# Performance work log

Hardware: AMD Instinct MI355X
Metric: run time of the kernel (lower is better)

Reference implementation:

```python
import jax, jax.numpy as jnp
import numpy as np

EPS = 1e-6
N_HEADS = 8


def causal_dot_product(q, k, v):
    # q,k: [n,h,l,d]; v: [n,h,l,m]
    kv = jnp.einsum('nhld,nhlm->nhldm', k, v)          # [n,h,l,d,m] (large, matches original)
    kv = jnp.cumsum(kv, axis=2)
    return jnp.einsum('nhld,nhldm->nhlm', q, kv)


def flow_attention_causal(queries, keys, values, Wq, bq, Wk, bk, Wv, bv, Wo, bo):
    B, L, _ = queries.shape
    H = N_HEADS
    # projections + split heads -> [B,H,L,Dh]
    def proj(x, W, b):
        y = x @ W + b
        return y.reshape(B, L, H, -1).transpose(0, 2, 1, 3)
    q = jax.nn.sigmoid(proj(queries, Wq, bq))
    k = jax.nn.sigmoid(proj(keys, Wk, bk))
    v = proj(values, Wv, bv)

    normal = (jnp.arange(L, dtype=q.dtype) + 1.0)[None, None, :]  # [1,1,L]

    sink_incoming = 1.0 / jnp.einsum('nhld,nhld->nhl', q + EPS, jnp.cumsum(k, axis=2) + EPS)
    source_outgoing = 1.0 / jnp.einsum('nhld,nhld->nhl', k + EPS, jnp.cumsum(q, axis=2) + EPS)
    sink_incoming = sink_incoming * normal
    source_outgoing = source_outgoing * normal

    conserved_sink = jnp.einsum('nhld,nhld->nhl', q + EPS,
                                jnp.cumsum(k * source_outgoing[..., None], axis=2) + EPS) / normal
    conserved_source = jnp.einsum('nhld,nhld->nhl', k + EPS,
                                  jnp.cumsum(q * sink_incoming[..., None], axis=2) + EPS) / normal
    conserved_source = jnp.clip(conserved_source, -1.0, 1.0)

    sink_allocation = jax.nn.sigmoid(conserved_sink)
    conserved_source = jnp.exp(conserved_source)
    source_competition = conserved_source / jnp.cumsum(conserved_source, axis=-1) * normal

    x = causal_dot_product(q * (sink_incoming / normal)[..., None],
                           k,
                           v * source_competition[..., None]) * sink_allocation[..., None]
    x = x.transpose(0, 2, 1, 3).reshape(B, L, -1)
    return x @ Wo + bo  # dropout is identity at eval


def setup_inputs() -> dict:
    key = jax.random.key(0)
    ks = jax.random.split(key, 11)
    B, L, Din, Dm, Dout = 2, 1024, 512, 512, 512
    s = 0.02
    return {
        'queries': jax.random.normal(ks[0], (B, L, Din), jnp.float32),
        'keys': jax.random.normal(ks[1], (B, L, Din), jnp.float32),
        'values': jax.random.normal(ks[2], (B, L, Din), jnp.float32),
        'Wq': jax.random.normal(ks[3], (Din, Dm), jnp.float32) * s,
        'bq': jnp.zeros((Dm,), jnp.float32),
        'Wk': jax.random.normal(ks[4], (Din, Dm), jnp.float32) * s,
        'bk': jnp.zeros((Dm,), jnp.float32),
        'Wv': jax.random.normal(ks[5], (Din, Dm), jnp.float32) * s,
        'bv': jnp.zeros((Dm,), jnp.float32),
        'Wo': jax.random.normal(ks[6], (Dm, Dout), jnp.float32) * s,
        'bo': jnp.zeros((Dout,), jnp.float32),
    }


def reference(queries, keys, values, Wq, bq, Wk, bk, Wv, bv, Wo, bo):
    return flow_attention_causal(queries, keys, values, Wq, bq, Wk, bk, Wv, bv, Wo, bo)
```

## Files before the change

kernel.cpp:

```cpp
#include <hip/hip_runtime.h>
#include <math.h>

#define EPSF 1e-6f

constexpr int B_  = 2;
constexpr int L_  = 1024;
constexpr int D_  = 512;
constexpr int H_  = 8;
constexpr int DH_ = 64;
constexpr int BL_ = B_ * L_;
constexpr int BH_ = B_ * H_;
constexpr int CT_ = 64;
constexpr int NC_ = L_ / CT_;

typedef __attribute__((ext_vector_type(8))) short bf16x8;
typedef __attribute__((ext_vector_type(4))) float f32x4;

__device__ __forceinline__ unsigned short f2bf(float f) {
  union { float f; unsigned int u; } v; v.f = f;
  const unsigned int u = v.u;
  return (unsigned short)((u + 0x7FFFu + ((u >> 16) & 1u)) >> 16);
}

__device__ __forceinline__ int sw(int row, int col) {
  return row * 64 + (col ^ ((row & 7) << 3));
}

__global__ __launch_bounds__(256) void proj3_k(const float* __restrict__ Qin,
                                               const float* __restrict__ Kin,
                                               const float* __restrict__ Vin,
                                               const float* __restrict__ Wq,
                                               const float* __restrict__ bq,
                                               const float* __restrict__ Wk,
                                               const float* __restrict__ bk,
                                               const float* __restrict__ Wv,
                                               const float* __restrict__ bv,
                                               float* __restrict__ Qb,
                                               float* __restrict__ Kb,
                                               float* __restrict__ Vb,
                                               float* __restrict__ sumQ,
                                               float* __restrict__ sumK) {
  const int z = blockIdx.z;
  const float* A    = (z == 0) ? Qin : (z == 1) ? Kin : Vin;
  const float* W    = (z == 0) ? Wq  : (z == 1) ? Wk  : Wv;
  const float* bias = (z == 0) ? bq  : (z == 1) ? bk  : bv;
  float* out        = (z == 0) ? Qb  : (z == 1) ? Kb  : Vb;
  float* csum       = (z == 0) ? sumQ : (z == 1) ? sumK : nullptr;
  const bool sig = (z < 2);

  __shared__ __align__(16) short Als[64 * 40];
  __shared__ __align__(16) short Bls[64 * 40];
  const int tid = threadIdx.x;
  const int m0 = blockIdx.x * 64, n0 = blockIdx.y * 64;
  const int arow = tid >> 2, akq = (tid & 3) << 3;
  const int bcol = tid & 63, bk0 = (tid >> 6) << 3;
  const int lane = tid & 63, wid = tid >> 6;
  const int wr = wid >> 1, wc = wid & 1;
  const int lrow = lane & 15, lk = (lane >> 4) << 3;

  f32x4 acc[2][2] = {{{0.f, 0.f, 0.f, 0.f}, {0.f, 0.f, 0.f, 0.f}},
                     {{0.f, 0.f, 0.f, 0.f}, {0.f, 0.f, 0.f, 0.f}}};
  float ra[8], rb[8];

  auto loadAB = [&](int kt) {
    const float4 f0 = *(const float4*)&A[(size_t)(m0 + arow) * D_ + kt + akq];
    const float4 f1 = *(const float4*)&A[(size_t)(m0 + arow) * D_ + kt + akq + 4];
    ra[0] = f0.x; ra[1] = f0.y; ra[2] = f0.z; ra[3] = f0.w;
    ra[4] = f1.x; ra[5] = f1.y; ra[6] = f1.z; ra[7] = f1.w;
    const float* gw = &W[(size_t)(kt + bk0) * D_ + n0 + bcol];
#pragma unroll
    for (int j = 0; j < 8; ++j) rb[j] = gw[(size_t)j * D_];
  };
  auto writeLDS = [&]() {
    bf16x8 pa, pb;
#pragma unroll
    for (int j = 0; j < 8; ++j) {
      pa[j] = (short)f2bf(ra[j]);
      pb[j] = (short)f2bf(rb[j]);
    }
    *(bf16x8*)&Als[arow * 40 + akq] = pa;
    *(bf16x8*)&Bls[bcol * 40 + bk0] = pb;
  };
  auto compute = [&]() {
    bf16x8 a0 = *(const bf16x8*)&Als[(wr * 32 + lrow) * 40 + lk];
    bf16x8 a1 = *(const bf16x8*)&Als[(wr * 32 + 16 + lrow) * 40 + lk];
    bf16x8 b0 = *(const bf16x8*)&Bls[(wc * 32 + lrow) * 40 + lk];
    bf16x8 b1 = *(const bf16x8*)&Bls[(wc * 32 + 16 + lrow) * 40 + lk];
    acc[0][0] = __builtin_amdgcn_mfma_f32_16x16x32_bf16(a0, b0, acc[0][0], 0, 0, 0);
    acc[0][1] = __builtin_amdgcn_mfma_f32_16x16x32_bf16(a0, b1, acc[0][1], 0, 0, 0);
    acc[1][0] = __builtin_amdgcn_mfma_f32_16x16x32_bf16(a1, b0, acc[1][0], 0, 0, 0);
    acc[1][1] = __builtin_amdgcn_mfma_f32_16x16x32_bf16(a1, b1, acc[1][1], 0, 0, 0);
  };

  loadAB(0);
  writeLDS();
  for (int kt = 32; kt < D_; kt += 32) {
    loadAB(kt);
    __syncthreads();
    compute();
    __syncthreads();
    writeLDS();
  }
  __syncthreads();
  compute();

  const int b = m0 >> 10, h = n0 >> 6;
  float psum[2] = {0.f, 0.f};
#pragma unroll
  for (int j = 0; j < 2; ++j) {
    const int col = n0 + wc * 32 + j * 16 + lrow;
    const float bv4 = bias[col];
    const int dh = col & 63;
#pragma unroll
    for (int i = 0; i < 2; ++i) {
#pragma unroll
      for (int r = 0; r < 4; ++r) {
        const int row = m0 + wr * 32 + i * 16 + (lane >> 4) * 4 + r;
        float x = acc[i][j][r] + bv4;
        if (sig) x = 1.0f / (1.0f + expf(-x));
        const int l = row & (L_ - 1);
        out[(((size_t)(b * H_ + h)) * L_ + l) * DH_ + dh] = x;
        psum[j] += x;
      }
    }
  }
  if (csum) {
    float* sumS = (float*)Als;
#pragma unroll
    for (int j = 0; j < 2; ++j) {
      psum[j] += __shfl_xor(psum[j], 16);
      psum[j] += __shfl_xor(psum[j], 32);
      if ((lane >> 4) == 0) sumS[wr * 64 + wc * 32 + j * 16 + lrow] = psum[j];
    }
    __syncthreads();
    if (tid < 64) {
      const int c = (m0 & (L_ - 1)) >> 6;
      const int bc = (b * H_ + h) * NC_ + c;
      csum[bc * DH_ + tid] = sumS[tid] + sumS[64 + tid];
    }
  }
}

__global__ __launch_bounds__(256) void flow_phase1_k(const float* __restrict__ Qb,
                                                     const float* __restrict__ Kb,
                                                     const float* __restrict__ sumQ,
                                                     const float* __restrict__ sumK,
                                                     float* __restrict__ qscale,
                                                     float* __restrict__ si_a,
                                                     float* __restrict__ so_a,
                                                     float* __restrict__ sumQSI,
                                                     float* __restrict__ sumKSO) {
  const int bc = blockIdx.x, bh = bc >> 4, c = bc & (NC_ - 1);
  const int g = bc * CT_;
  const int tid = threadIdx.x, lane = tid & 63, w = tid >> 6;
  __shared__ float qS[64][65], kS[64][65];
  __shared__ float pqS[64], pkS[64];
  __shared__ float aS[4][64], bS[4][64];
  __shared__ float siS[64], soS[64];
  for (int i = tid; i < CT_ * DH_; i += 256) {
    const int row = i >> 6, d = i & 63;
    qS[row][d] = Qb[(size_t)g * DH_ + i];
    kS[row][d] = Kb[(size_t)g * DH_ + i];
  }
  if (tid < 64) {
    float pq = 0.f, pk = 0.f;
    for (int cc = 0; cc < c; ++cc) {
      pq += sumQ[(bh * NC_ + cc) * DH_ + tid];
      pk += sumK[(bh * NC_ + cc) * DH_ + tid];
    }
    pqS[tid] = pq; pkS[tid] = pk;
  }
  __syncthreads();
  float ap = 0.f, bp = 0.f;
  for (int dd = 0; dd < 16; ++dd) {
    const int d = w * 16 + dd;
    const float qv = qS[lane][d];
    const float kv = kS[lane][d];
    float ck = kv, cq = qv;
#pragma unroll
    for (int off = 1; off < 64; off <<= 1) {
      const float t1 = __shfl_up(ck, off);
      const float t2 = __shfl_up(cq, off);
      ck += (lane >= off) ? t1 : 0.f;
      cq += (lane >= off) ? t2 : 0.f;
    }
    ck += pkS[d];
    cq += pqS[d];
    ap += (qv + EPSF) * (ck + EPSF);
    bp += (kv + EPSF) * (cq + EPSF);
  }
  aS[w][lane] = ap; bS[w][lane] = bp;
  __syncthreads();
  const float normal = (float)(c * CT_ + lane + 1);
  if (w == 0) {
    const float a = aS[0][lane] + aS[1][lane] + aS[2][lane] + aS[3][lane];
    const float b = bS[0][lane] + bS[1][lane] + bS[2][lane] + bS[3][lane];
    const float si = normal / a, so = normal / b;
    qscale[g + lane] = 1.0f / a;
    si_a[g + lane] = si;
    so_a[g + lane] = so;
    siS[lane] = si; soS[lane] = so;
  }
  __syncthreads();
  float sq = 0.f, sk = 0.f;
#pragma unroll
  for (int li = 0; li < 16; ++li) {
    const int l = w * 16 + li;
    sq += qS[l][lane] * siS[l];
    sk += kS[l][lane] * soS[l];
  }
  aS[w][lane] = sq; bS[w][lane] = sk;
  __syncthreads();
  if (tid < 64) {
    sumQSI[bc * DH_ + tid] = aS[0][tid] + aS[1][tid] + aS[2][tid] + aS[3][tid];
    sumKSO[bc * DH_ + tid] = bS[0][tid] + bS[1][tid] + bS[2][tid] + bS[3][tid];
  }
}

__global__ __launch_bounds__(256) void flow_phase2_k(const float* __restrict__ Qb,
                                                     const float* __restrict__ Kb,
                                                     const float* __restrict__ sumQSI,
                                                     const float* __restrict__ sumKSO,
                                                     const float* __restrict__ si_a,
                                                     const float* __restrict__ so_a,
                                                     float* __restrict__ salloc,
                                                     float* __restrict__ e_a,
                                                     float* __restrict__ sumE) {
  const int bc = blockIdx.x, bh = bc >> 4, c = bc & (NC_ - 1);
  const int g = bc * CT_;
  const int tid = threadIdx.x, lane = tid & 63, w = tid >> 6;
  __shared__ float qS[64][65], kS[64][65];
  __shared__ float pqS[64], pkS[64];
  __shared__ float aS[4][64], bS[4][64];
  for (int i = tid; i < CT_ * DH_; i += 256) {
    const int row = i >> 6, d = i & 63;
    qS[row][d] = Qb[(size_t)g * DH_ + i];
    kS[row][d] = Kb[(size_t)g * DH_ + i];
  }
  if (tid < 64) {
    float pq = 0.f, pk = 0.f;
    for (int cc = 0; cc < c; ++cc) {
      pq += sumQSI[(bh * NC_ + cc) * DH_ + tid];
      pk += sumKSO[(bh * NC_ + cc) * DH_ + tid];
    }
    pqS[tid] = pq; pkS[tid] = pk;
  }
  __syncthreads();
  const float si = si_a[g + lane];
  const float so = so_a[g + lane];
  float c1p = 0.f, c2p = 0.f;
  for (int dd = 0; dd < 16; ++dd) {
    const int d = w * 16 + dd;
    const float qv = qS[lane][d];
    const float kv = kS[lane][d];
    float ckso = kv * so, cqsi = qv * si;
#pragma unroll
    for (int off = 1; off < 64; off <<= 1) {
      const float t1 = __shfl_up(ckso, off);
      const float t2 = __shfl_up(cqsi, off);
      ckso += (lane >= off) ? t1 : 0.f;
      cqsi += (lane >= off) ? t2 : 0.f;
    }
    ckso += pkS[d];
    cqsi += pqS[d];
    c1p += (qv + EPSF) * (ckso + EPSF);
    c2p += (kv + EPSF) * (cqsi + EPSF);
  }
  aS[w][lane] = c1p; bS[w][lane] = c2p;
  __syncthreads();
  if (w == 0) {
    const float c1 = aS[0][lane] + aS[1][lane] + aS[2][lane] + aS[3][lane];
    const float c2 = bS[0][lane] + bS[1][lane] + bS[2][lane] + bS[3][lane];
    const float normal = (float)(c * CT_ + lane + 1);
    const float cs_sink = c1 / normal;
    salloc[g + lane] = 1.0f / (1.0f + expf(-cs_sink));
    float cs_src = c2 / normal;
    cs_src = fminf(1.0f, fmaxf(-1.0f, cs_src));
    const float e = expf(cs_src);
    e_a[g + lane] = e;
    float tot = e;
#pragma unroll
    for (int off = 32; off; off >>= 1) tot += __shfl_xor(tot, off);
    if (lane == 0) sumE[bc] = tot;
  }
}

__global__ __launch_bounds__(256) void flow_ckv_k(const float* __restrict__ K,
                                                  const float* __restrict__ V,
                                                  const float* __restrict__ e_a,
                                                  const float* __restrict__ sumE,
                                                  float* __restrict__ comp,
                                                  float* __restrict__ KV) {
  const int bc = blockIdx.x, bh = bc >> 4, c = bc & (NC_ - 1);
  const int g = bc * CT_;
  const int tid = threadIdx.x;
  __shared__ float compS[CT_];
  __shared__ float kb[CT_][DH_];
  __shared__ float vb[CT_][DH_];
  if (tid < 64) {
    const int lane = tid;
    const float e = e_a[g + lane];
    float se = (lane < c) ? sumE[bh * NC_ + lane] : 0.f;
#pragma unroll
    for (int off = 32; off; off >>= 1) se += __shfl_xor(se, off);
    float s = e;
#pragma unroll
    for (int off = 1; off < 64; off <<= 1) {
      const float t = __shfl_up(s, off);
      s += (lane >= off) ? t : 0.f;
    }
    const float cf = e / (se + s) * (float)(c * CT_ + lane + 1);
    compS[lane] = cf;
    comp[g + lane] = cf;
  }
  __syncthreads();
  const float* k = K + (size_t)g * DH_;
  const float* v = V + (size_t)g * DH_;
  for (int i = tid; i < CT_ * DH_; i += 256) {
    const int l = i >> 6;
    kb[l][i & 63] = k[i];
    vb[l][i & 63] = v[i] * compS[l];
  }
  __syncthreads();
  const int m = tid & 63, dg = tid >> 6;
  float acc[16] = {};
  for (int l = 0; l < CT_; ++l) {
    const float vm = vb[l][m];
#pragma unroll
    for (int i = 0; i < 16; ++i) acc[i] += kb[l][dg * 16 + i] * vm;
  }
  float* out = KV + ((size_t)bc * DH_ + dg * 16) * DH_ + m;
#pragma unroll
  for (int i = 0; i < 16; ++i) out[i * DH_] = acc[i];
}

__global__ __launch_bounds__(256) void kv_prefix_k(float* __restrict__ KV) {
  const int idx = blockIdx.x * 256 + threadIdx.x;
  const int bh = idx >> 12, p = idx & 4095;
  const size_t base = (size_t)bh * NC_ * DH_ * DH_ + p;
  float run = 0.f;
#pragma unroll
  for (int c = 0; c < NC_; ++c) {
    const float t = KV[base + (size_t)c * DH_ * DH_];
    KV[base + (size_t)c * DH_ * DH_] = run;
    run += t;
  }
}

__global__ __launch_bounds__(256) void attn_k(const float* __restrict__ Q,
                                              const float* __restrict__ K,
                                              const float* __restrict__ V,
                                              const float* __restrict__ KVp,
                                              const float* __restrict__ qscale,
                                              const float* __restrict__ salloc,
                                              const float* __restrict__ comp,
                                              unsigned short* __restrict__ X) {
  const int bc = blockIdx.x;
  const int bh = bc >> 4, c = bc & (NC_ - 1);
  const int bb = bh >> 3, hh = bh & (H_ - 1);
  const int g = bc * CT_;
  __shared__ __align__(16) unsigned short qp16[64 * 64];
  __shared__ __align__(16) unsigned short k16[64 * 64];
  __shared__ __align__(16) unsigned short vT16[64 * 64];
  __shared__ __align__(16) unsigned short kvT16[64 * 64];
  __shared__ __align__(16) unsigned short S16[64 * 64];
  const int tid = threadIdx.x;
  for (int i = tid; i < 64 * 64; i += 256) {
    const int r = i >> 6, d = i & 63;
    qp16[sw(r, d)] = f2bf(Q[(size_t)g * DH_ + i] * qscale[g + r]);
    k16[sw(r, d)] = f2bf(K[(size_t)g * DH_ + i]);
    vT16[sw(d, r)] = f2bf(V[(size_t)g * DH_ + i] * comp[g + r]);
    kvT16[sw(d, r)] = f2bf(KVp[(size_t)bc * DH_ * DH_ + i]);
  }
  __syncthreads();

  const int lane = tid & 63, w = tid >> 6;
  const int fr = lane & 15, fk = (lane >> 4) << 3;
  const int arow = w * 16 + fr;
  f32x4 accX[4] = {{0.f, 0.f, 0.f, 0.f}, {0.f, 0.f, 0.f, 0.f},
                   {0.f, 0.f, 0.f, 0.f}, {0.f, 0.f, 0.f, 0.f}};
  f32x4 accS[4] = {{0.f, 0.f, 0.f, 0.f}, {0.f, 0.f, 0.f, 0.f},
                   {0.f, 0.f, 0.f, 0.f}, {0.f, 0.f, 0.f, 0.f}};

  const bf16x8 aq0 = *(const bf16x8*)&qp16[sw(arow, fk)];
  const bf16x8 aq1 = *(const bf16x8*)&qp16[sw(arow, fk + 32)];
#pragma unroll
  for (int cb = 0; cb < 4; ++cb) {
    const int bcol = cb * 16 + fr;
    const bf16x8 bv0 = *(const bf16x8*)&kvT16[sw(bcol, fk)];
    const bf16x8 bv1 = *(const bf16x8*)&kvT16[sw(bcol, fk + 32)];
    accX[cb] = __builtin_amdgcn_mfma_f32_16x16x32_bf16(aq0, bv0, accX[cb], 0, 0, 0);
    accX[cb] = __builtin_amdgcn_mfma_f32_16x16x32_bf16(aq1, bv1, accX[cb], 0, 0, 0);
    const bf16x8 bk0 = *(const bf16x8*)&k16[sw(bcol, fk)];
    const bf16x8 bk1 = *(const bf16x8*)&k16[sw(bcol, fk + 32)];
    accS[cb] = __builtin_amdgcn_mfma_f32_16x16x32_bf16(aq0, bk0, accS[cb], 0, 0, 0);
    accS[cb] = __builtin_amdgcn_mfma_f32_16x16x32_bf16(aq1, bk1, accS[cb], 0, 0, 0);
  }
#pragma unroll
  for (int cb = 0; cb < 4; ++cb) {
#pragma unroll
    for (int r = 0; r < 4; ++r) {
      const int l = w * 16 + (lane >> 4) * 4 + r;
      const int j = cb * 16 + fr;
      S16[sw(l, j)] = (j <= l) ? f2bf(accS[cb][r]) : (unsigned short)0;
    }
  }
  __syncthreads();
  const bf16x8 as0 = *(const bf16x8*)&S16[sw(arow, fk)];
  const bf16x8 as1 = *(const bf16x8*)&S16[sw(arow, fk + 32)];
#pragma unroll
  for (int cb = 0; cb < 4; ++cb) {
    const int bcol = cb * 16 + fr;
    const bf16x8 bv0 = *(const bf16x8*)&vT16[sw(bcol, fk)];
    const bf16x8 bv1 = *(const bf16x8*)&vT16[sw(bcol, fk + 32)];
    accX[cb] = __builtin_amdgcn_mfma_f32_16x16x32_bf16(as0, bv0, accX[cb], 0, 0, 0);
    accX[cb] = __builtin_amdgcn_mfma_f32_16x16x32_bf16(as1, bv1, accX[cb], 0, 0, 0);
  }
#pragma unroll
  for (int r = 0; r < 4; ++r) {
    const int l = w * 16 + (lane >> 4) * 4 + r;
    const float sal = salloc[g + l];
    const size_t rowbase = ((size_t)(bb * L_ + c * CT_ + l)) * D_ + hh * DH_;
#pragma unroll
    for (int cb = 0; cb < 4; ++cb) {
      const int m = cb * 16 + fr;
      X[rowbase + m] = f2bf(accX[cb][r] * sal);
    }
  }
}

__global__ __launch_bounds__(256) void gemm_out_k(const unsigned short* __restrict__ A,
                                                  const float* __restrict__ W,
                                                  const float* __restrict__ bias,
                                                  float* __restrict__ out) {
  __shared__ __align__(16) short Als[64 * 40];
  __shared__ __align__(16) short Bls[64 * 40];
  const int tid = threadIdx.x;
  const int m0 = blockIdx.x * 64, n0 = blockIdx.y * 64;
  const int arow = tid >> 2, akq = (tid & 3) << 3;
  const int bcol = tid & 63, bk0 = (tid >> 6) << 3;
  const int lane = tid & 63, wid = tid >> 6;
  const int wr = wid >> 1, wc = wid & 1;
  const int lrow = lane & 15, lk = (lane >> 4) << 3;

  f32x4 acc[2][2] = {{{0.f, 0.f, 0.f, 0.f}, {0.f, 0.f, 0.f, 0.f}},
                     {{0.f, 0.f, 0.f, 0.f}, {0.f, 0.f, 0.f, 0.f}}};
  bf16x8 pa;
  float rb[8];
  auto loadAB = [&](int kt) {
    pa = *(const bf16x8*)&A[(size_t)(m0 + arow) * D_ + kt + akq];
    const float* gw = &W[(size_t)(kt + bk0) * D_ + n0 + bcol];
#pragma unroll
    for (int j = 0; j < 8; ++j) rb[j] = gw[(size_t)j * D_];
  };
  auto writeLDS = [&]() {
    bf16x8 pb;
#pragma unroll
    for (int j = 0; j < 8; ++j) pb[j] = (short)f2bf(rb[j]);
    *(bf16x8*)&Als[arow * 40 + akq] = pa;
    *(bf16x8*)&Bls[bcol * 40 + bk0] = pb;
  };
  auto compute = [&]() {
    bf16x8 a0 = *(const bf16x8*)&Als[(wr * 32 + lrow) * 40 + lk];
    bf16x8 a1 = *(const bf16x8*)&Als[(wr * 32 + 16 + lrow) * 40 + lk];
    bf16x8 b0 = *(const bf16x8*)&Bls[(wc * 32 + lrow) * 40 + lk];
    bf16x8 b1 = *(const bf16x8*)&Bls[(wc * 32 + 16 + lrow) * 40 + lk];
    acc[0][0] = __builtin_amdgcn_mfma_f32_16x16x32_bf16(a0, b0, acc[0][0], 0, 0, 0);
    acc[0][1] = __builtin_amdgcn_mfma_f32_16x16x32_bf16(a0, b1, acc[0][1], 0, 0, 0);
    acc[1][0] = __builtin_amdgcn_mfma_f32_16x16x32_bf16(a1, b0, acc[1][0], 0, 0, 0);
    acc[1][1] = __builtin_amdgcn_mfma_f32_16x16x32_bf16(a1, b1, acc[1][1], 0, 0, 0);
  };

  loadAB(0);
  writeLDS();
  for (int kt = 32; kt < D_; kt += 32) {
    loadAB(kt);
    __syncthreads();
    compute();
    __syncthreads();
    writeLDS();
  }
  __syncthreads();
  compute();

#pragma unroll
  for (int j = 0; j < 2; ++j) {
    const int col = n0 + wc * 32 + j * 16 + lrow;
    const float bv4 = bias[col];
#pragma unroll
    for (int i = 0; i < 2; ++i) {
#pragma unroll
      for (int r = 0; r < 4; ++r) {
        const int row = m0 + wr * 32 + i * 16 + (lane >> 4) * 4 + r;
        out[(size_t)row * D_ + col] = acc[i][j][r] + bv4;
      }
    }
  }
}

extern "C" void kernel_launch(void* const* d_in, const int* in_sizes, int n_in,
                              void* d_out, int out_size, void* d_ws, size_t ws_size,
                              hipStream_t stream) {
  (void)in_sizes; (void)n_in; (void)out_size; (void)ws_size;
  const float* queries = (const float*)d_in[0];
  const float* keys    = (const float*)d_in[1];
  const float* values  = (const float*)d_in[2];
  const float* Wq = (const float*)d_in[3];
  const float* bq = (const float*)d_in[4];
  const float* Wk = (const float*)d_in[5];
  const float* bk = (const float*)d_in[6];
  const float* Wv = (const float*)d_in[7];
  const float* bv = (const float*)d_in[8];
  const float* Wo = (const float*)d_in[9];
  const float* bo = (const float*)d_in[10];

  float* ws = (float*)d_ws;
  const size_t seg = (size_t)BH_ * L_ * DH_;
  float* Qb  = ws;
  float* Kb  = Qb + seg;
  float* Vb  = Kb + seg;
  float* KVb = Vb + seg;
  float* p   = KVb + (size_t)BH_ * NC_ * DH_ * DH_;
  float* qscale = p; p += BH_ * L_;
  float* salloc = p; p += BH_ * L_;
  float* comp   = p; p += BH_ * L_;
  float* si_a   = p; p += BH_ * L_;
  float* so_a   = p; p += BH_ * L_;
  float* e_a    = p; p += BH_ * L_;
  float* sumQ   = p; p += BH_ * NC_ * DH_;
  float* sumK   = p; p += BH_ * NC_ * DH_;
  float* sumQSI = p; p += BH_ * NC_ * DH_;
  float* sumKSO = p; p += BH_ * NC_ * DH_;
  float* sumE   = p; p += BH_ * NC_;
  unsigned short* Xb16 = (unsigned short*)p;

  proj3_k<<<dim3(BL_ / 64, D_ / 64, 3), 256, 0, stream>>>(
      queries, keys, values, Wq, bq, Wk, bk, Wv, bv, Qb, Kb, Vb, sumQ, sumK);
  flow_phase1_k<<<BH_ * NC_, 256, 0, stream>>>(Qb, Kb, sumQ, sumK,
                                               qscale, si_a, so_a, sumQSI, sumKSO);
  flow_phase2_k<<<BH_ * NC_, 256, 0, stream>>>(Qb, Kb, sumQSI, sumKSO, si_a, so_a,
                                               salloc, e_a, sumE);
  flow_ckv_k<<<BH_ * NC_, 256, 0, stream>>>(Kb, Vb, e_a, sumE, comp, KVb);
  kv_prefix_k<<<BH_ * NC_, 256, 0, stream>>>(KVb);
  attn_k<<<BH_ * NC_, 256, 0, stream>>>(Qb, Kb, Vb, KVb, qscale, salloc, comp, Xb16);
  gemm_out_k<<<dim3(BL_ / 64, D_ / 64), 256, 0, stream>>>(Xb16, Wo, bo, (float*)d_out);
}
```

Baseline: 68.50 us.

## Enlarge projection GEMM tiles and fold KV prefix sum into attention kernel

The QKV projection GEMM moves to 128x128 tiles with 4x4 MFMA fragments per wave, and the output GEMM to 64x128 tiles, to raise data reuse per LDS load. The separate kv_prefix kernel is removed; each attention block now sums the preceding chunks' KV states itself using masked float4 loads over all chunks. This saves one launch and a read/write pass over the KV buffer, but has every attention block re-read the whole per-head KV array, and the larger GEMM tiles cut the grid size, which can lower occupancy.

```diff
diff --git a/kernel.cpp b/kernel.cpp
--- a/kernel.cpp
+++ b/kernel.cpp
@@ -48,48 +48,61 @@
   float* csum       = (z == 0) ? sumQ : (z == 1) ? sumK : nullptr;
   const bool sig = (z < 2);
 
-  __shared__ __align__(16) short Als[64 * 40];
-  __shared__ __align__(16) short Bls[64 * 40];
+  __shared__ __align__(16) short Als[128 * 40];
+  __shared__ __align__(16) short Bls[128 * 40];
   const int tid = threadIdx.x;
-  const int m0 = blockIdx.x * 64, n0 = blockIdx.y * 64;
-  const int arow = tid >> 2, akq = (tid & 3) << 3;
-  const int bcol = tid & 63, bk0 = (tid >> 6) << 3;
+  const int m0 = blockIdx.x * 128, n0 = blockIdx.y * 128;
+  const int arow = tid >> 1, ak0 = (tid & 1) << 4;
+  const int bcol = tid & 127, bk0 = (tid >> 7) << 4;
   const int lane = tid & 63, wid = tid >> 6;
   const int wr = wid >> 1, wc = wid & 1;
-  const int lrow = lane & 15, lk = (lane >> 4) << 3;
-
-  f32x4 acc[2][2] = {{{0.f, 0.f, 0.f, 0.f}, {0.f, 0.f, 0.f, 0.f}},
-                     {{0.f, 0.f, 0.f, 0.f}, {0.f, 0.f, 0.f, 0.f}}};
-  float ra[8], rb[8];
+  const int fr = lane & 15, lk = (lane >> 4) << 3;
+
+  f32x4 acc[4][4];
+#pragma unroll
+  for (int i = 0; i < 4; ++i)
+#pragma unroll
+    for (int j = 0; j < 4; ++j) acc[i][j] = {0.f, 0.f, 0.f, 0.f};
+  float ra[16], rb[16];
 
   auto loadAB = [&](int kt) {
-    const float4 f0 = *(const float4*)&A[(size_t)(m0 + arow) * D_ + kt + akq];
-    const float4 f1 = *(const float4*)&A[(size_t)(m0 + arow) * D_ + kt + akq + 4];
-    ra[0] = f0.x; ra[1] = f0.y; ra[2] = f0.z; ra[3] = f0.w;
-    ra[4] = f1.x; ra[5] = f1.y; ra[6] = f1.z; ra[7] = f1.w;
+#pragma unroll
+    for (int j = 0; j < 4; ++j) {
+      const float4 f = *(const float4*)&A[(size_t)(m0 + arow) * D_ + kt + ak0 + 4 * j];
+      ra[4 * j + 0] = f.x; ra[4 * j + 1] = f.y; ra[4 * j + 2] = f.z; ra[4 * j + 3] = f.w;
+    }
     const float* gw = &W[(size_t)(kt + bk0) * D_ + n0 + bcol];
 #pragma unroll
-    for (int j = 0; j < 8; ++j) rb[j] = gw[(size_t)j * D_];
+    for (int j = 0; j < 16; ++j) rb[j] = gw[(size_t)j * D_];
   };
   auto writeLDS = [&]() {
-    bf16x8 pa, pb;
+    bf16x8 pa0, pa1, pb0, pb1;
 #pragma unroll
     for (int j = 0; j < 8; ++j) {
-      pa[j] = (short)f2bf(ra[j]);
-      pb[j] = (short)f2bf(rb[j]);
-    }
-    *(bf16x8*)&Als[arow * 40 + akq] = pa;
-    *(bf16x8*)&Bls[bcol * 40 + bk0] = pb;
+      pa0[j] = (short)f2bf(ra[j]);
+      pa1[j] = (short)f2bf(ra[j + 8]);
+      pb0[j] = (short)f2bf(rb[j]);
+      pb1[j] = (short)f2bf(rb[j + 8]);
+    }
+    *(bf16x8*)&Als[arow * 40 + ak0] = pa0;
+    *(bf16x8*)&Als[arow * 40 + ak0 + 8] = pa1;
+    *(bf16x8*)&Bls[bcol * 40 + bk0] = pb0;
+    *(bf16x8*)&Bls[bcol * 40 + bk0 + 8] = pb1;
   };
   auto compute = [&]() {
-    bf16x8 a0 = *(const bf16x8*)&Als[(wr * 32 + lrow) * 40 + lk];
-    bf16x8 a1 = *(const bf16x8*)&Als[(wr * 32 + 16 + lrow) * 40 + lk];
-    bf16x8 b0 = *(const bf16x8*)&Bls[(wc * 32 + lrow) * 40 + lk];
-    bf16x8 b1 = *(const bf16x8*)&Bls[(wc * 32 + 16 + lrow) * 40 + lk];
-    acc[0][0] = __builtin_amdgcn_mfma_f32_16x16x32_bf16(a0, b0, acc[0][0], 0, 0, 0);
-    acc[0][1] = __builtin_amdgcn_mfma_f32_16x16x32_bf16(a0, b1, acc[0][1], 0, 0, 0);
-    acc[1][0] = __builtin_amdgcn_mfma_f32_16x16x32_bf16(a1, b0, acc[1][0], 0, 0, 0);
-    acc[1][1] = __builtin_amdgcn_mfma_f32_16x16x32_bf16(a1, b1, acc[1][1], 0, 0, 0);
+    bf16x8 af[4], bf[4];
+#pragma unroll
+    for (int mb = 0; mb < 4; ++mb)
+      af[mb] = *(const bf16x8*)&Als[(wr * 64 + mb * 16 + fr) * 40 + lk];
+#pragma unroll
+    for (int nb = 0; nb < 4; ++nb)
+      bf[nb] = *(const bf16x8*)&Bls[(wc * 64 + nb * 16 + fr) * 40 + lk];
+#pragma unroll
+    for (int mb = 0; mb < 4; ++mb)
+#pragma unroll
+      for (int nb = 0; nb < 4; ++nb)
+        acc[mb][nb] = __builtin_amdgcn_mfma_f32_16x16x32_bf16(af[mb], bf[nb],
+                                                              acc[mb][nb], 0, 0, 0);
   };
 
   loadAB(0);
@@ -104,39 +117,36 @@
   __syncthreads();
   compute();
 
-  const int b = m0 >> 10, h = n0 >> 6;
-  float psum[2] = {0.f, 0.f};
-#pragma unroll
-  for (int j = 0; j < 2; ++j) {
-    const int col = n0 + wc * 32 + j * 16 + lrow;
-    const float bv4 = bias[col];
-    const int dh = col & 63;
-#pragma unroll
-    for (int i = 0; i < 2; ++i) {
+  const int b = m0 >> 10;
+  const int h = (n0 + wc * 64) >> 6;
+  const int cch = ((m0 & (L_ - 1)) + wr * 64) >> 6;
+  float psum[4] = {0.f, 0.f, 0.f, 0.f};
+#pragma unroll
+  for (int nb = 0; nb < 4; ++nb) {
+    const int dh = nb * 16 + fr;
+    const float bv4 = bias[(h << 6) + dh];
+#pragma unroll
+    for (int mb = 0; mb < 4; ++mb) {
 #pragma unroll
       for (int r = 0; r < 4; ++r) {
-        const int row = m0 + wr * 32 + i * 16 + (lane >> 4) * 4 + r;
-        float x = acc[i][j][r] + bv4;
+        const int l = (m0 & (L_ - 1)) + wr * 64 + mb * 16 + (lane >> 4) * 4 + r;
+        float x = acc[mb][nb][r] + bv4;
         if (sig) x = 1.0f / (1.0f + expf(-x));
-        const int l = row & (L_ - 1);
         out[(((size_t)(b * H_ + h)) * L_ + l) * DH_ + dh] = x;
-        psum[j] += x;
+        psum[nb] += x;
       }
     }
   }
   if (csum) {
-    float* sumS = (float*)Als;
-#pragma unroll
-    for (int j = 0; j < 2; ++j) {
-      psum[j] += __shfl_xor(psum[j], 16);
-      psum[j] += __shfl_xor(psum[j], 32);
-      if ((lane >> 4) == 0) sumS[wr * 64 + wc * 32 + j * 16 + lrow] = psum[j];
-    }
-    __syncthreads();
-    if (tid < 64) {
-      const int c = (m0 & (L_ - 1)) >> 6;
-      const int bc = (b * H_ + h) * NC_ + c;
-      csum[bc * DH_ + tid] = sumS[tid] + sumS[64 + tid];
+#pragma unroll
+    for (int nb = 0; nb < 4; ++nb) {
+      psum[nb] += __shfl_xor(psum[nb], 16);
+      psum[nb] += __shfl_xor(psum[nb], 32);
+    }
+    if ((lane >> 4) == 0) {
+      const int bc = (b * H_ + h) * NC_ + cch;
+#pragma unroll
+      for (int nb = 0; nb < 4; ++nb) csum[bc * DH_ + nb * 16 + fr] = psum[nb];
     }
   }
 }
@@ -334,23 +344,10 @@
   for (int i = 0; i < 16; ++i) out[i * DH_] = acc[i];
 }
 
-__global__ __launch_bounds__(256) void kv_prefix_k(float* __restrict__ KV) {
-  const int idx = blockIdx.x * 256 + threadIdx.x;
-  const int bh = idx >> 12, p = idx & 4095;
-  const size_t base = (size_t)bh * NC_ * DH_ * DH_ + p;
-  float run = 0.f;
-#pragma unroll
-  for (int c = 0; c < NC_; ++c) {
-    const float t = KV[base + (size_t)c * DH_ * DH_];
-    KV[base + (size_t)c * DH_ * DH_] = run;
-    run += t;
-  }
-}
-
 __global__ __launch_bounds__(256) void attn_k(const float* __restrict__ Q,
                                               const float* __restrict__ K,
                                               const float* __restrict__ V,
-                                              const float* __restrict__ KVp,
+                                              const float* __restrict__ KVraw,
                                               const float* __restrict__ qscale,
                                               const float* __restrict__ salloc,
                                               const float* __restrict__ comp,
@@ -370,7 +367,23 @@
     qp16[sw(r, d)] = f2bf(Q[(size_t)g * DH_ + i] * qscale[g + r]);
     k16[sw(r, d)] = f2bf(K[(size_t)g * DH_ + i]);
     vT16[sw(d, r)] = f2bf(V[(size_t)g * DH_ + i] * comp[g + r]);
-    kvT16[sw(d, r)] = f2bf(KVp[(size_t)bc * DH_ * DH_ + i]);
+  }
+  {
+    const float* kvbh = KVraw + (size_t)bh * NC_ * DH_ * DH_;
+    for (int i4 = tid; i4 < DH_ * DH_ / 4; i4 += 256) {
+      const int d = i4 >> 4, mg = (i4 & 15) << 2;
+      float s0 = 0.f, s1 = 0.f, s2 = 0.f, s3 = 0.f;
+#pragma unroll
+      for (int cc = 0; cc < NC_; ++cc) {
+        const float4 t = *(const float4*)&kvbh[(size_t)cc * (DH_ * DH_) + d * DH_ + mg];
+        const float msk = (cc < c) ? 1.f : 0.f;
+        s0 += t.x * msk; s1 += t.y * msk; s2 += t.z * msk; s3 += t.w * msk;
+      }
+      kvT16[sw(mg + 0, d)] = f2bf(s0);
+      kvT16[sw(mg + 1, d)] = f2bf(s1);
+      kvT16[sw(mg + 2, d)] = f2bf(s2);
+      kvT16[sw(mg + 3, d)] = f2bf(s3);
+    }
   }
   __syncthreads();
 
@@ -434,41 +447,53 @@
                                                   const float* __restrict__ bias,
                                                   float* __restrict__ out) {
   __shared__ __align__(16) short Als[64 * 40];
-  __shared__ __align__(16) short Bls[64 * 40];
+  __shared__ __align__(16) short Bls[128 * 40];
   const int tid = threadIdx.x;
-  const int m0 = blockIdx.x * 64, n0 = blockIdx.y * 64;
-  const int arow = tid >> 2, akq = (tid & 3) << 3;
-  const int bcol = tid & 63, bk0 = (tid >> 6) << 3;
+  const int m0 = blockIdx.x * 64, n0 = blockIdx.y * 128;
+  const int arow = tid >> 2, ak0 = (tid & 3) << 3;
+  const int bcol = tid & 127, bk0 = (tid >> 7) << 4;
   const int lane = tid & 63, wid = tid >> 6;
   const int wr = wid >> 1, wc = wid & 1;
-  const int lrow = lane & 15, lk = (lane >> 4) << 3;
-
-  f32x4 acc[2][2] = {{{0.f, 0.f, 0.f, 0.f}, {0.f, 0.f, 0.f, 0.f}},
-                     {{0.f, 0.f, 0.f, 0.f}, {0.f, 0.f, 0.f, 0.f}}};
+  const int fr = lane & 15, lk = (lane >> 4) << 3;
+
+  f32x4 acc[2][4];
+#pragma unroll
+  for (int i = 0; i < 2; ++i)
+#pragma unroll
+    for (int j = 0; j < 4; ++j) acc[i][j] = {0.f, 0.f, 0.f, 0.f};
   bf16x8 pa;
-  float rb[8];
+  float rb[16];
   auto loadAB = [&](int kt) {
-    pa = *(const bf16x8*)&A[(size_t)(m0 + arow) * D_ + kt + akq];
+    pa = *(const bf16x8*)&A[(size_t)(m0 + arow) * D_ + kt + ak0];
     const float* gw = &W[(size_t)(kt + bk0) * D_ + n0 + bcol];
 #pragma unroll
-    for (int j = 0; j < 8; ++j) rb[j] = gw[(size_t)j * D_];
+    for (int j = 0; j < 16; ++j) rb[j] = gw[(size_t)j * D_];
   };
   auto writeLDS = [&]() {
-    bf16x8 pb;
-#pragma unroll
-    for (int j = 0; j < 8; ++j) pb[j] = (short)f2bf(rb[j]);
-    *(bf16x8*)&Als[arow * 40 + akq] = pa;
-    *(bf16x8*)&Bls[bcol * 40 + bk0] = pb;
+    bf16x8 pb0, pb1;
+#pragma unroll
+    for (int j = 0; j < 8; ++j) {
+      pb0[j] = (short)f2bf(rb[j]);
+      pb1[j] = (short)f2bf(rb[j + 8]);
+    }
+    *(bf16x8*)&Als[arow * 40 + ak0] = pa;
+    *(bf16x8*)&Bls[bcol * 40 + bk0] = pb0;
+    *(bf16x8*)&Bls[bcol * 40 + bk0 + 8] = pb1;
   };
   auto compute = [&]() {
-    bf16x8 a0 = *(const bf16x8*)&Als[(wr * 32 + lrow) * 40 + lk];
-    bf16x8 a1 = *(const bf16x8*)&Als[(wr * 32 + 16 + lrow) * 40 + lk];
-    bf16x8 b0 = *(const bf16x8*)&Bls[(wc * 32 + lrow) * 40 + lk];
-    bf16x8 b1 = *(const bf16x8*)&Bls[(wc * 32 + 16 + lrow) * 40 + lk];
-    acc[0][0] = __builtin_amdgcn_mfma_f32_16x16x32_bf16(a0, b0, acc[0][0], 0, 0, 0);
-    acc[0][1] = __builtin_amdgcn_mfma_f32_16x16x32_bf16(a0, b1, acc[0][1], 0, 0, 0);
-    acc[1][0] = __builtin_amdgcn_mfma_f32_16x16x32_bf16(a1, b0, acc[1][0], 0, 0, 0);
-    acc[1][1] = __builtin_amdgcn_mfma_f32_16x16x32_bf16(a1, b1, acc[1][1], 0, 0, 0);
+    bf16x8 af[2], bf[4];
+#pragma unroll
+    for (int mb = 0; mb < 2; ++mb)
+      af[mb] = *(const bf16x8*)&Als[(wr * 32 + mb * 16 + fr) * 40 + lk];
+#pragma unroll
+    for (int nb = 0; nb < 4; ++nb)
+      bf[nb] = *(const bf16x8*)&Bls[(wc * 64 + nb * 16 + fr) * 40 + lk];
+#pragma unroll
+    for (int mb = 0; mb < 2; ++mb)
+#pragma unroll
+      for (int nb = 0; nb < 4; ++nb)
+        acc[mb][nb] = __builtin_amdgcn_mfma_f32_16x16x32_bf16(af[mb], bf[nb],
+                                                              acc[mb][nb], 0, 0, 0);
   };
 
   loadAB(0);
@@ -484,15 +509,15 @@
   compute();
 
 #pragma unroll
-  for (int j = 0; j < 2; ++j) {
-    const int col = n0 + wc * 32 + j * 16 + lrow;
+  for (int nb = 0; nb < 4; ++nb) {
+    const int col = n0 + wc * 64 + nb * 16 + fr;
     const float bv4 = bias[col];
 #pragma unroll
-    for (int i = 0; i < 2; ++i) {
+    for (int mb = 0; mb < 2; ++mb) {
 #pragma unroll
       for (int r = 0; r < 4; ++r) {
-        const int row = m0 + wr * 32 + i * 16 + (lane >> 4) * 4 + r;
-        out[(size_t)row * D_ + col] = acc[i][j][r] + bv4;
+        const int row = m0 + wr * 32 + mb * 16 + (lane >> 4) * 4 + r;
+        out[(size_t)row * D_ + col] = acc[mb][nb][r] + bv4;
       }
     }
   }
@@ -534,14 +559,13 @@
   float* sumE   = p; p += BH_ * NC_;
   unsigned short* Xb16 = (unsigned short*)p;
 
-  proj3_k<<<dim3(BL_ / 64, D_ / 64, 3), 256, 0, stream>>>(
+  proj3_k<<<dim3(BL_ / 128, D_ / 128, 3), 256, 0, stream>>>(
       queries, keys, values, Wq, bq, Wk, bk, Wv, bv, Qb, Kb, Vb, sumQ, sumK);
   flow_phase1_k<<<BH_ * NC_, 256, 0, stream>>>(Qb, Kb, sumQ, sumK,
                                                qscale, si_a, so_a, sumQSI, sumKSO);
   flow_phase2_k<<<BH_ * NC_, 256, 0, stream>>>(Qb, Kb, sumQSI, sumKSO, si_a, so_a,
                                                salloc, e_a, sumE);
   flow_ckv_k<<<BH_ * NC_, 256, 0, stream>>>(Kb, Vb, e_a, sumE, comp, KVb);
-  kv_prefix_k<<<BH_ * NC_, 256, 0, stream>>>(KVb);
   attn_k<<<BH_ * NC_, 256, 0, stream>>>(Qb, Kb, Vb, KVb, qscale, salloc, comp, Xb16);
-  gemm_out_k<<<dim3(BL_ / 64, D_ / 64), 256, 0, stream>>>(Xb16, Wo, bo, (float*)d_out);
-}
+  gemm_out_k<<<dim3(BL_ / 64, D_ / 128), 256, 0, stream>>>(Xb16, Wo, bo, (float*)d_out);
+}
```

Measured after the change: 83.55 us. 22.0% more time.

## Store projected Q/K/V as bf16 and use MFMA for chunk KV outer products

Applied to the files above, without the earlier changes.

The projection kernel now writes Q, K and V intermediates as bf16 instead of fp32, and the chunk sums are taken from the rounded values. The downstream phase, chunk-KV and attention kernels load them with 16-byte vector loads and widen to float where needed. The per-chunk K^T·V accumulation moves from a scalar FMA loop to bf16 MFMA instructions. The aim is to halve intermediate memory traffic and speed up the KV build, at the cost of extra bf16 rounding in the flow normalisation statistics.

```diff
diff --git a/kernel.cpp b/kernel.cpp
--- a/kernel.cpp
+++ b/kernel.cpp
@@ -21,6 +21,10 @@
   const unsigned int u = v.u;
   return (unsigned short)((u + 0x7FFFu + ((u >> 16) & 1u)) >> 16);
 }
+__device__ __forceinline__ float bf2f(unsigned short u) {
+  union { unsigned int u; float f; } v; v.u = ((unsigned int)u) << 16;
+  return v.f;
+}
 
 __device__ __forceinline__ int sw(int row, int col) {
   return row * 64 + (col ^ ((row & 7) << 3));
@@ -35,16 +39,16 @@
                                                const float* __restrict__ bk,
                                                const float* __restrict__ Wv,
                                                const float* __restrict__ bv,
-                                               float* __restrict__ Qb,
-                                               float* __restrict__ Kb,
-                                               float* __restrict__ Vb,
+                                               unsigned short* __restrict__ Qb,
+                                               unsigned short* __restrict__ Kb,
+                                               unsigned short* __restrict__ Vb,
                                                float* __restrict__ sumQ,
                                                float* __restrict__ sumK) {
   const int z = blockIdx.z;
   const float* A    = (z == 0) ? Qin : (z == 1) ? Kin : Vin;
   const float* W    = (z == 0) ? Wq  : (z == 1) ? Wk  : Wv;
   const float* bias = (z == 0) ? bq  : (z == 1) ? bk  : bv;
-  float* out        = (z == 0) ? Qb  : (z == 1) ? Kb  : Vb;
+  unsigned short* out = (z == 0) ? Qb : (z == 1) ? Kb : Vb;
   float* csum       = (z == 0) ? sumQ : (z == 1) ? sumK : nullptr;
   const bool sig = (z < 2);
 
@@ -118,9 +122,10 @@
         const int row = m0 + wr * 32 + i * 16 + (lane >> 4) * 4 + r;
         float x = acc[i][j][r] + bv4;
         if (sig) x = 1.0f / (1.0f + expf(-x));
+        const unsigned short ub = f2bf(x);
         const int l = row & (L_ - 1);
-        out[(((size_t)(b * H_ + h)) * L_ + l) * DH_ + dh] = x;
-        psum[j] += x;
+        out[(((size_t)(b * H_ + h)) * L_ + l) * DH_ + dh] = ub;
+        psum[j] += bf2f(ub);
       }
     }
   }
@@ -141,8 +146,8 @@
   }
 }
 
-__global__ __launch_bounds__(256) void flow_phase1_k(const float* __restrict__ Qb,
-                                                     const float* __restrict__ Kb,
+__global__ __launch_bounds__(256) void flow_phase1_k(const unsigned short* __restrict__ Qb,
+                                                     const unsigned short* __restrict__ Kb,
                                                      const float* __restrict__ sumQ,
                                                      const float* __restrict__ sumK,
                                                      float* __restrict__ qscale,
@@ -157,10 +162,17 @@
   __shared__ float pqS[64], pkS[64];
   __shared__ float aS[4][64], bS[4][64];
   __shared__ float siS[64], soS[64];
-  for (int i = tid; i < CT_ * DH_; i += 256) {
-    const int row = i >> 6, d = i & 63;
-    qS[row][d] = Qb[(size_t)g * DH_ + i];
-    kS[row][d] = Kb[(size_t)g * DH_ + i];
+#pragma unroll
+  for (int it = 0; it < 2; ++it) {
+    const int i8 = it * 256 + tid;
+    const int row = i8 >> 3, d0 = (i8 & 7) << 3;
+    const bf16x8 qv = *(const bf16x8*)&Qb[(size_t)g * DH_ + i8 * 8];
+    const bf16x8 kv = *(const bf16x8*)&Kb[(size_t)g * DH_ + i8 * 8];
+#pragma unroll
+    for (int j = 0; j < 8; ++j) {
+      qS[row][d0 + j] = bf2f((unsigned short)qv[j]);
+      kS[row][d0 + j] = bf2f((unsigned short)kv[j]);
+    }
   }
   if (tid < 64) {
     float pq = 0.f, pk = 0.f;
@@ -217,8 +229,8 @@
   }
 }
 
-__global__ __launch_bounds__(256) void flow_phase2_k(const float* __restrict__ Qb,
-                                                     const float* __restrict__ Kb,
+__global__ __launch_bounds__(256) void flow_phase2_k(const unsigned short* __restrict__ Qb,
+                                                     const unsigned short* __restrict__ Kb,
                                                      const float* __restrict__ sumQSI,
                                                      const float* __restrict__ sumKSO,
                                                      const float* __restrict__ si_a,
@@ -232,10 +244,17 @@
   __shared__ float qS[64][65], kS[64][65];
   __shared__ float pqS[64], pkS[64];
   __shared__ float aS[4][64], bS[4][64];
-  for (int i = tid; i < CT_ * DH_; i += 256) {
-    const int row = i >> 6, d = i & 63;
-    qS[row][d] = Qb[(size_t)g * DH_ + i];
-    kS[row][d] = Kb[(size_t)g * DH_ + i];
+#pragma unroll
+  for (int it = 0; it < 2; ++it) {
+    const int i8 = it * 256 + tid;
+    const int row = i8 >> 3, d0 = (i8 & 7) << 3;
+    const bf16x8 qv = *(const bf16x8*)&Qb[(size_t)g * DH_ + i8 * 8];
+    const bf16x8 kv = *(const bf16x8*)&Kb[(size_t)g * DH_ + i8 * 8];
+#pragma unroll
+    for (int j = 0; j < 8; ++j) {
+      qS[row][d0 + j] = bf2f((unsigned short)qv[j]);
+      kS[row][d0 + j] = bf2f((unsigned short)kv[j]);
+    }
   }
   if (tid < 64) {
     float pq = 0.f, pk = 0.f;
@@ -285,8 +304,8 @@
   }
 }
 
-__global__ __launch_bounds__(256) void flow_ckv_k(const float* __restrict__ K,
-                                                  const float* __restrict__ V,
+__global__ __launch_bounds__(256) void flow_ckv_k(const unsigned short* __restrict__ K16,
+                                                  const unsigned short* __restrict__ V16,
                                                   const float* __restrict__ e_a,
                                                   const float* __restrict__ sumE,
                                                   float* __restrict__ comp,
@@ -295,8 +314,8 @@
   const int g = bc * CT_;
   const int tid = threadIdx.x;
   __shared__ float compS[CT_];
-  __shared__ float kb[CT_][DH_];
-  __shared__ float vb[CT_][DH_];
+  __shared__ __align__(16) unsigned short kT16[64 * 64];
+  __shared__ __align__(16) unsigned short vT16[64 * 64];
   if (tid < 64) {
     const int lane = tid;
     const float e = e_a[g + lane];
@@ -314,24 +333,40 @@
     comp[g + lane] = cf;
   }
   __syncthreads();
-  const float* k = K + (size_t)g * DH_;
-  const float* v = V + (size_t)g * DH_;
-  for (int i = tid; i < CT_ * DH_; i += 256) {
-    const int l = i >> 6;
-    kb[l][i & 63] = k[i];
-    vb[l][i & 63] = v[i] * compS[l];
-  }
-  __syncthreads();
-  const int m = tid & 63, dg = tid >> 6;
-  float acc[16] = {};
-  for (int l = 0; l < CT_; ++l) {
-    const float vm = vb[l][m];
-#pragma unroll
-    for (int i = 0; i < 16; ++i) acc[i] += kb[l][dg * 16 + i] * vm;
-  }
-  float* out = KV + ((size_t)bc * DH_ + dg * 16) * DH_ + m;
-#pragma unroll
-  for (int i = 0; i < 16; ++i) out[i * DH_] = acc[i];
+#pragma unroll
+  for (int it = 0; it < 2; ++it) {
+    const int i8 = it * 256 + tid;
+    const int l = i8 >> 3, d0 = (i8 & 7) << 3;
+    const bf16x8 kv = *(const bf16x8*)&K16[(size_t)g * DH_ + i8 * 8];
+    const bf16x8 vv = *(const bf16x8*)&V16[(size_t)g * DH_ + i8 * 8];
+    const float cl = compS[l];
+#pragma unroll
+    for (int j = 0; j < 8; ++j) {
+      kT16[sw(d0 + j, l)] = (unsigned short)kv[j];
+      vT16[sw(d0 + j, l)] = f2bf(bf2f((unsigned short)vv[j]) * cl);
+    }
+  }
+  __syncthreads();
+  const int lane = tid & 63, w = tid >> 6;
+  const int fr = lane & 15, fk = (lane >> 4) << 3;
+  f32x4 acc[4] = {{0.f, 0.f, 0.f, 0.f}, {0.f, 0.f, 0.f, 0.f},
+                  {0.f, 0.f, 0.f, 0.f}, {0.f, 0.f, 0.f, 0.f}};
+  const bf16x8 a0 = *(const bf16x8*)&kT16[sw(w * 16 + fr, fk)];
+  const bf16x8 a1 = *(const bf16x8*)&kT16[sw(w * 16 + fr, fk + 32)];
+#pragma unroll
+  for (int cb = 0; cb < 4; ++cb) {
+    const bf16x8 b0 = *(const bf16x8*)&vT16[sw(cb * 16 + fr, fk)];
+    const bf16x8 b1 = *(const bf16x8*)&vT16[sw(cb * 16 + fr, fk + 32)];
+    acc[cb] = __builtin_amdgcn_mfma_f32_16x16x32_bf16(a0, b0, acc[cb], 0, 0, 0);
+    acc[cb] = __builtin_amdgcn_mfma_f32_16x16x32_bf16(a1, b1, acc[cb], 0, 0, 0);
+  }
+  float* outp = KV + (size_t)bc * DH_ * DH_;
+#pragma unroll
+  for (int r = 0; r < 4; ++r) {
+    const int d = w * 16 + (lane >> 4) * 4 + r;
+#pragma unroll
+    for (int cb = 0; cb < 4; ++cb) outp[d * DH_ + cb * 16 + fr] = acc[cb][r];
+  }
 }
 
 __global__ __launch_bounds__(256) void kv_prefix_k(float* __restrict__ KV) {
@@ -347,9 +382,9 @@
   }
 }
 
-__global__ __launch_bounds__(256) void attn_k(const float* __restrict__ Q,
-                                              const float* __restrict__ K,
-                                              const float* __restrict__ V,
+__global__ __launch_bounds__(256) void attn_k(const unsigned short* __restrict__ Q16,
+                                              const unsigned short* __restrict__ K16,
+                                              const unsigned short* __restrict__ V16,
                                               const float* __restrict__ KVp,
                                               const float* __restrict__ qscale,
                                               const float* __restrict__ salloc,
@@ -365,12 +400,31 @@
   __shared__ __align__(16) unsigned short kvT16[64 * 64];
   __shared__ __align__(16) unsigned short S16[64 * 64];
   const int tid = threadIdx.x;
-  for (int i = tid; i < 64 * 64; i += 256) {
-    const int r = i >> 6, d = i & 63;
-    qp16[sw(r, d)] = f2bf(Q[(size_t)g * DH_ + i] * qscale[g + r]);
-    k16[sw(r, d)] = f2bf(K[(size_t)g * DH_ + i]);
-    vT16[sw(d, r)] = f2bf(V[(size_t)g * DH_ + i] * comp[g + r]);
-    kvT16[sw(d, r)] = f2bf(KVp[(size_t)bc * DH_ * DH_ + i]);
+#pragma unroll
+  for (int it = 0; it < 2; ++it) {
+    const int i8 = it * 256 + tid;
+    const int r = i8 >> 3, d0 = (i8 & 7) << 3;
+    const bf16x8 qv = *(const bf16x8*)&Q16[(size_t)g * DH_ + i8 * 8];
+    const bf16x8 kv = *(const bf16x8*)&K16[(size_t)g * DH_ + i8 * 8];
+    const bf16x8 vv = *(const bf16x8*)&V16[(size_t)g * DH_ + i8 * 8];
+    const float qs = qscale[g + r];
+    const float cl = comp[g + r];
+    bf16x8 pq;
+#pragma unroll
+    for (int j = 0; j < 8; ++j) pq[j] = (short)f2bf(bf2f((unsigned short)qv[j]) * qs);
+    *(bf16x8*)&qp16[sw(r, d0)] = pq;
+    *(bf16x8*)&k16[sw(r, d0)] = kv;
+#pragma unroll
+    for (int j = 0; j < 8; ++j)
+      vT16[sw(d0 + j, r)] = f2bf(bf2f((unsigned short)vv[j]) * cl);
+  }
+  for (int i4 = tid; i4 < DH_ * DH_ / 4; i4 += 256) {
+    const int d = i4 >> 4, m0 = (i4 & 15) << 2;
+    const float4 t = *(const float4*)&KVp[(size_t)bc * DH_ * DH_ + d * DH_ + m0];
+    kvT16[sw(m0 + 0, d)] = f2bf(t.x);
+    kvT16[sw(m0 + 1, d)] = f2bf(t.y);
+    kvT16[sw(m0 + 2, d)] = f2bf(t.z);
+    kvT16[sw(m0 + 3, d)] = f2bf(t.w);
   }
   __syncthreads();
 
@@ -514,12 +568,11 @@
   const float* Wo = (const float*)d_in[9];
   const float* bo = (const float*)d_in[10];
 
-  float* ws = (float*)d_ws;
   const size_t seg = (size_t)BH_ * L_ * DH_;
-  float* Qb  = ws;
-  float* Kb  = Qb + seg;
-  float* Vb  = Kb + seg;
-  float* KVb = Vb + seg;
+  unsigned short* Qb = (unsigned short*)d_ws;
+  unsigned short* Kb = Qb + seg;
+  unsigned short* Vb = Kb + seg;
+  float* KVb = (float*)(Vb + seg);
   float* p   = KVb + (size_t)BH_ * NC_ * DH_ * DH_;
   float* qscale = p; p += BH_ * L_;
   float* salloc = p; p += BH_ * L_;
```

Result: faster. 62.66 us (-8.5%).
